# Kernel optimization log

Measured on AMD Instinct MI355X. Metric: run time of the kernel, lower is better.

## Reference

```python
import jax, jax.numpy as jnp
import numpy as np

NB, B, C, L = 4, 16, 256, 4096
BN_EPS = 1e-5


def setup_inputs() -> dict:
    key = jax.random.key(0)
    ks = jax.random.split(key, 10)
    s = 0.02
    return {
        "x": jax.random.normal(ks[0], (NB, B, C, L), jnp.float32),
        "Wq": jax.random.normal(ks[1], (NB, C, C), jnp.float32) * s,
        "bq": jax.random.normal(ks[2], (NB, C), jnp.float32) * s,
        "Wk": jax.random.normal(ks[3], (NB, C, C), jnp.float32) * s,
        "bk": jax.random.normal(ks[4], (NB, C), jnp.float32) * s,
        "Wv": jax.random.normal(ks[5], (NB, C, C), jnp.float32) * s,
        "bv": jax.random.normal(ks[6], (NB, C), jnp.float32) * s,
        "Wo": jax.random.normal(ks[7], (NB, C, C), jnp.float32) * s,
        "bo": jax.random.normal(ks[8], (NB, C), jnp.float32) * s,
        "gamma": jnp.ones((NB, C), jnp.float32),
        "beta": jnp.zeros((NB, C), jnp.float32),
        "edge_w": jnp.ones((NB, NB), jnp.float32),
        "branch_imp": jnp.ones((NB,), jnp.float32),
    }


def _proj(W, b, x):
    # 1x1 Conv1d == per-branch channel mixing: [nb,o,c] x [nb,B,c,L] -> [nb,B,o,L]
    return jnp.einsum('noc,nbcl->nbol', W, x) + b[:, None, :, None]


def reference(x, Wq, bq, Wk, bk, Wv, bv, Wo, bo, gamma, beta, edge_w, branch_imp):
    feat_dim = x.shape[2]
    scale = jnp.sqrt(jnp.asarray(feat_dim, x.dtype))
    q = _proj(Wq, bq, x)
    k = _proj(Wk, bk, x)
    v = _proj(Wv, bv, x)
    # descriptors: [nb, B, C, 2] = (mean over L, max over L)
    qd = jnp.stack([q.mean(axis=-1), q.max(axis=-1)], axis=-1)
    kd = jnp.stack([k.mean(axis=-1), k.max(axis=-1)], axis=-1)
    # mean over 2x2 bmm entries == (sum_p qd)(sum_q kd) summed over C, / 4
    scores = jnp.einsum('ibcp,jbcq->ijb', qd, kd) / (4.0 * scale)
    scores = scores * edge_w[:, :, None]
    attn = jax.nn.softmax(scores, axis=1) * jax.nn.softmax(branch_imp)[None, :, None]
    # weighted aggregation over source branches j
    agg = jnp.einsum('ijb,jbcl->ibcl', attn, v)
    out = _proj(Wo, bo, agg)
    # BatchNorm1d (training-mode batch statistics over B and L per channel, per branch)
    mean = out.mean(axis=(1, 3), keepdims=True)
    var = out.var(axis=(1, 3), keepdims=True)
    bn = (out - mean) * jax.lax.rsqrt(var + BN_EPS)
    bn = bn * gamma[:, None, :, None] + beta[:, None, :, None]
    return jax.nn.relu(bn) + x
```

## Files before the change

kernel.cpp:

```cpp
#include <hip/hip_runtime.h>
#include <stdint.h>
#include <stddef.h>

#define NBR 4
#define BSZ 16
#define CHN 256
#define LEN 4096
#define NB_B 64
#define BL   65536
#define BN_EPS 1e-5f
#define W_EL (NBR*CHN*CHN)

typedef unsigned short ushortT;
typedef unsigned short ushort4_t __attribute__((ext_vector_type(4)));
typedef unsigned short ushort8_t __attribute__((ext_vector_type(8)));
typedef short bf16x8 __attribute__((ext_vector_type(8)));
typedef float f32x4 __attribute__((ext_vector_type(4)));

__device__ __forceinline__ float bf2f(ushortT u) {
    return __uint_as_float(((unsigned)u) << 16);
}
__device__ __forceinline__ ushortT f2bf(float f) {
    unsigned b = __float_as_uint(f);
    return (ushortT)((b + 0x7FFFu + ((b >> 16) & 1u)) >> 16);
}
__device__ __forceinline__ unsigned encf(float f) {
    unsigned b = __float_as_uint(f);
    return (b & 0x80000000u) ? ~b : (b | 0x80000000u);
}
__device__ __forceinline__ float decf(unsigned u) {
    unsigned b = (u & 0x80000000u) ? (u ^ 0x80000000u) : ~u;
    return __uint_as_float(b);
}

__device__ __forceinline__ int swzX(int row, int cb) {
    return row * 512 + (cb ^ ((row & 7) << 4) ^ (((row >> 3) & 3) << 7));
}
__device__ __forceinline__ int swzW(int row, int cb) {
    return row * 128 + (cb ^ ((row & 7) << 4));
}

template <bool BF16IN>
__device__ __forceinline__ void stage_x(const void* act, ushortT* sX, int z, int lbase, int tid)
{
    const int ls = tid & 127;
    const int gh = tid >> 7;
    if (BF16IN) {
        const ushortT* xp = (const ushortT*)act + (size_t)z * CHN * LEN + lbase + ls;
#pragma unroll
        for (int g = 0; g < 16; ++g) {
            int c0 = (gh * 16 + g) * 8;
            ushort8_t u;
#pragma unroll
            for (int i = 0; i < 8; ++i) u[i] = xp[(size_t)(c0 + i) * LEN];
            *(ushort8_t*)((char*)sX + swzX(ls, c0 * 2)) = u;
        }
    } else {
        const float* xp = (const float*)act + (size_t)z * CHN * LEN + lbase + ls;
#pragma unroll
        for (int g = 0; g < 16; ++g) {
            int c0 = (gh * 16 + g) * 8;
            ushort8_t u;
#pragma unroll
            for (int i = 0; i < 8; ++i) u[i] = f2bf(xp[(size_t)(c0 + i) * LEN]);
            *(ushort8_t*)((char*)sX + swzX(ls, c0 * 2)) = u;
        }
    }
}

__device__ __forceinline__ void stage_w(const ushortT* Wb, ushortT* sW, int obase, int kb, int tid)
{
    const int r = tid >> 1;
    const int h = tid & 1;
    const ushortT* wp = Wb + (size_t)(obase + r) * CHN + kb + h * 32;
#pragma unroll
    for (int i = 0; i < 4; ++i) {
        ushort8_t u = *(const ushort8_t*)(wp + i * 8);
        *(ushort8_t*)((char*)sW + swzW(r, h * 64 + i * 16)) = u;
    }
}

__device__ __forceinline__ void mfma_chunk(const ushortT* sX, const ushortT* sW,
                                           f32x4 acc[4][4], int wr, int wc, int lane, int kb)
{
    const int am = wr * 64 + (lane & 15);
    const int bo = wc * 64 + (lane & 15);
    const int kg = (lane >> 4) * 16;
#pragma unroll
    for (int s = 0; s < 2; ++s) {
        bf16x8 a[4], b[4];
#pragma unroll
        for (int mf = 0; mf < 4; ++mf)
            a[mf] = *(const bf16x8*)((const char*)sX + swzX(am + mf * 16, kb * 2 + s * 64 + kg));
#pragma unroll
        for (int nf = 0; nf < 4; ++nf)
            b[nf] = *(const bf16x8*)((const char*)sW + swzW(bo + nf * 16, s * 64 + kg));
#pragma unroll
        for (int mf = 0; mf < 4; ++mf)
#pragma unroll
            for (int nf = 0; nf < 4; ++nf)
                acc[mf][nf] = __builtin_amdgcn_mfma_f32_16x16x32_bf16(a[mf], b[nf], acc[mf][nf], 0, 0, 0);
    }
}

__global__ __launch_bounds__(256, 2)
void qkv_kernel(const float* __restrict__ x, const ushortT* __restrict__ Wbf,
                const float* __restrict__ bv,
                float* __restrict__ qsum, unsigned* __restrict__ qmax,
                float* __restrict__ ksum, unsigned* __restrict__ kmax,
                ushortT* __restrict__ vbuf)
{
    __shared__ ushortT sX[128 * 256];
    __shared__ ushortT sW[128 * 64];
    const int tid = threadIdx.x;
    const int lane = tid & 63;
    const int wv = tid >> 6;
    const int wr = wv >> 1, wc = wv & 1;
    const int lbase = blockIdx.x * 128;
    const int z = blockIdx.y;
    const int n = z >> 4;

    stage_x<false>(x, sX, z, lbase, tid);

    for (int w = 0; w < 3; ++w) {
        const ushortT* Wb = Wbf + ((size_t)w * NBR + n) * CHN * CHN;
        for (int ot = 0; ot < 2; ++ot) {
            const int obase = ot * 128;
            f32x4 acc[4][4];
            const f32x4 z4 = {0.f, 0.f, 0.f, 0.f};
#pragma unroll
            for (int mf = 0; mf < 4; ++mf)
#pragma unroll
                for (int nf = 0; nf < 4; ++nf) acc[mf][nf] = z4;

            for (int kb = 0; kb < 4; ++kb) {
                __syncthreads();
                stage_w(Wb, sW, obase, kb * 64, tid);
                __syncthreads();
                mfma_chunk(sX, sW, acc, wr, wc, lane, kb * 64);
            }

            if (w < 2) {
                float* rs = (w == 0) ? qsum : ksum;
                unsigned* rm = (w == 0) ? qmax : kmax;
#pragma unroll
                for (int nf = 0; nf < 4; ++nf) {
                    float s = 0.f, m = -3.4e38f;
#pragma unroll
                    for (int mf = 0; mf < 4; ++mf)
#pragma unroll
                        for (int r = 0; r < 4; ++r) {
                            float v = acc[mf][nf][r];
                            s += v; m = fmaxf(m, v);
                        }
                    s += __shfl_xor(s, 16); s += __shfl_xor(s, 32);
                    m = fmaxf(m, __shfl_xor(m, 16)); m = fmaxf(m, __shfl_xor(m, 32));
                    if (lane < 16) {
                        int o = obase + wc * 64 + nf * 16 + lane;
                        atomicAdd(&rs[z * CHN + o], s);
                        atomicMax(&rm[z * CHN + o], encf(m));
                    }
                }
            } else {
#pragma unroll
                for (int nf = 0; nf < 4; ++nf) {
                    int o = obase + wc * 64 + nf * 16 + (lane & 15);
                    float bvv = bv[n * CHN + o];
#pragma unroll
                    for (int mf = 0; mf < 4; ++mf) {
                        int l = lbase + wr * 64 + mf * 16 + ((lane >> 4) << 2);
                        ushort4_t u;
#pragma unroll
                        for (int r = 0; r < 4; ++r) u[r] = f2bf(acc[mf][nf][r] + bvv);
                        *(ushort4_t*)(vbuf + (size_t)(z * CHN + o) * LEN + l) = u;
                    }
                }
            }
        }
    }
}

__global__ __launch_bounds__(256, 2)
void ogemm_kernel(const ushortT* __restrict__ agg, const ushortT* __restrict__ Wbo,
                  const float* __restrict__ bo_,
                  float* __restrict__ bnsum, float* __restrict__ bnss,
                  ushortT* __restrict__ outpre)
{
    __shared__ ushortT sX[128 * 256];
    __shared__ ushortT sW[128 * 64];
    const int tid = threadIdx.x;
    const int lane = tid & 63;
    const int wv = tid >> 6;
    const int wr = wv >> 1, wc = wv & 1;
    const int lbase = blockIdx.x * 128;
    const int z = blockIdx.y;
    const int n = z >> 4;
    const ushortT* Wb = Wbo + (size_t)n * CHN * CHN;

    stage_x<true>(agg, sX, z, lbase, tid);

    for (int ot = 0; ot < 2; ++ot) {
        const int obase = ot * 128;
        f32x4 acc[4][4];
        const f32x4 z4 = {0.f, 0.f, 0.f, 0.f};
#pragma unroll
        for (int mf = 0; mf < 4; ++mf)
#pragma unroll
            for (int nf = 0; nf < 4; ++nf) acc[mf][nf] = z4;

        for (int kb = 0; kb < 4; ++kb) {
            __syncthreads();
            stage_w(Wb, sW, obase, kb * 64, tid);
            __syncthreads();
            mfma_chunk(sX, sW, acc, wr, wc, lane, kb * 64);
        }

#pragma unroll
        for (int nf = 0; nf < 4; ++nf) {
            int o = obase + wc * 64 + nf * 16 + (lane & 15);
            float bb = bo_[n * CHN + o];
            float s = 0.f, q2 = 0.f;
#pragma unroll
            for (int mf = 0; mf < 4; ++mf) {
                int l = lbase + wr * 64 + mf * 16 + ((lane >> 4) << 2);
                ushort4_t u;
#pragma unroll
                for (int r = 0; r < 4; ++r) {
                    float v = acc[mf][nf][r] + bb;
                    u[r] = f2bf(v);
                    s += v; q2 += v * v;
                }
                *(ushort4_t*)(outpre + (size_t)(z * CHN + o) * LEN + l) = u;
            }
            s += __shfl_xor(s, 16); s += __shfl_xor(s, 32);
            q2 += __shfl_xor(q2, 16); q2 += __shfl_xor(q2, 32);
            if (lane < 16) {
                atomicAdd(&bnsum[n * CHN + o], s);
                atomicAdd(&bnss[n * CHN + o], q2);
            }
        }
    }
}

__global__ void wcvt_kernel(const float* __restrict__ Wq, const float* __restrict__ Wk,
                            const float* __restrict__ Wv, const float* __restrict__ Wo,
                            ushortT* __restrict__ Wbf)
{
    int t = blockIdx.x * 256 + threadIdx.x;
    const int per = W_EL / 4;
    if (t < 4 * per) {
        const float* srcs[4] = {Wq, Wk, Wv, Wo};
        int w = t / per;
        int r = t - w * per;
        float4 f = *(const float4*)(srcs[w] + (size_t)r * 4);
        ushort4_t u = {f2bf(f.x), f2bf(f.y), f2bf(f.z), f2bf(f.w)};
        *(ushort4_t*)(Wbf + (size_t)w * W_EL + (size_t)r * 4) = u;
    }
}

__global__ void attn_kernel(const float* __restrict__ qsum, const unsigned* __restrict__ qmax,
                            const float* __restrict__ ksum, const unsigned* __restrict__ kmax,
                            const float* __restrict__ bq, const float* __restrict__ bk,
                            const float* __restrict__ edge, const float* __restrict__ bimp,
                            float* __restrict__ attn)
{
    __shared__ float sc[NBR][NBR][BSZ];
    int tid = threadIdx.x;
    int i = tid >> 6, j = (tid >> 4) & 3, b = tid & 15;
    float s = 0.f;
    const float invL = 1.0f / (float)LEN;
    for (int c = 0; c < CHN; ++c) {
        int qi = (i * BSZ + b) * CHN + c;
        int ki = (j * BSZ + b) * CHN + c;
        float sq = qsum[qi] * invL + decf(qmax[qi]) + 2.f * bq[i * CHN + c];
        float sk = ksum[ki] * invL + decf(kmax[ki]) + 2.f * bk[j * CHN + c];
        s += sq * sk;
    }
    sc[i][j][b] = s * edge[i * 4 + j] * (1.0f / 64.0f);
    __syncthreads();
    if (tid < 64) {
        int ii = tid >> 4, bb = tid & 15;
        float m = -3.4e38f;
        for (int jj = 0; jj < 4; ++jj) m = fmaxf(m, sc[ii][jj][bb]);
        float e[4]; float sum = 0.f;
        for (int jj = 0; jj < 4; ++jj) { e[jj] = __expf(sc[ii][jj][bb] - m); sum += e[jj]; }
        float bm = fmaxf(fmaxf(bimp[0], bimp[1]), fmaxf(bimp[2], bimp[3]));
        float be[4]; float bs = 0.f;
        for (int jj = 0; jj < 4; ++jj) { be[jj] = __expf(bimp[jj] - bm); bs += be[jj]; }
        for (int jj = 0; jj < 4; ++jj)
            attn[(ii * 4 + jj) * BSZ + bb] = (e[jj] / sum) * (be[jj] / bs);
    }
}

__global__ __launch_bounds__(256)
void agg_kernel(const ushortT* __restrict__ v, const float* __restrict__ attn,
                ushortT* __restrict__ agg)
{
    __shared__ float sa[256];
    sa[threadIdx.x] = attn[threadIdx.x];
    __syncthreads();
    const long long U = (long long)BSZ * CHN * (LEN / 8);
    for (long long u = (long long)blockIdx.x * blockDim.x + threadIdx.x; u < U;
         u += (long long)gridDim.x * blockDim.x) {
        int l0 = (int)(u & 511) * 8;
        int c  = (int)(u >> 9) & 255;
        int b  = (int)(u >> 17);
        float vv[4][8];
#pragma unroll
        for (int j = 0; j < 4; ++j) {
            ushort8_t raw = *(const ushort8_t*)(v + (((size_t)(j * BSZ + b) * CHN + c) * LEN) + l0);
#pragma unroll
            for (int e = 0; e < 8; ++e) vv[j][e] = bf2f(raw[e]);
        }
#pragma unroll
        for (int i = 0; i < 4; ++i) {
            float a0 = sa[(i * 4 + 0) * BSZ + b];
            float a1 = sa[(i * 4 + 1) * BSZ + b];
            float a2 = sa[(i * 4 + 2) * BSZ + b];
            float a3 = sa[(i * 4 + 3) * BSZ + b];
            ushort8_t out;
#pragma unroll
            for (int e = 0; e < 8; ++e) {
                float r = a0 * vv[0][e] + a1 * vv[1][e] + a2 * vv[2][e] + a3 * vv[3][e];
                out[e] = f2bf(r);
            }
            *(ushort8_t*)(agg + (((size_t)(i * BSZ + b) * CHN + c) * LEN) + l0) = out;
        }
    }
}

__global__ void bnfin_kernel(const float* __restrict__ bnsum, const float* __restrict__ bnss,
                             const float* __restrict__ gamma, const float* __restrict__ beta,
                             float* __restrict__ scl, float* __restrict__ shf)
{
    int t = blockIdx.x * blockDim.x + threadIdx.x;
    if (t < NBR * CHN) {
        const float inv = 1.0f / (float)BL;
        float mean = bnsum[t] * inv;
        float var = bnss[t] * inv - mean * mean;
        float rs = rsqrtf(var + BN_EPS);
        float s = gamma[t] * rs;
        scl[t] = s;
        shf[t] = beta[t] - mean * s;
    }
}

__global__ __launch_bounds__(256)
void final_kernel(const ushortT* __restrict__ outpre, const float* __restrict__ x,
                  const float* __restrict__ scl, const float* __restrict__ shf,
                  float* __restrict__ out)
{
    const long long U = (long long)NB_B * CHN * (LEN / 8);
    for (long long u = (long long)blockIdx.x * blockDim.x + threadIdx.x; u < U;
         u += (long long)gridDim.x * blockDim.x) {
        int l0 = (int)(u & 511) * 8;
        int c  = (int)(u >> 9) & 255;
        int zz = (int)(u >> 17);
        int n  = zz >> 4;
        size_t base = ((size_t)zz * CHN + c) * LEN + l0;
        ushort8_t op = *(const ushort8_t*)(outpre + base);
        float4 x0 = *(const float4*)(x + base);
        float4 x1 = *(const float4*)(x + base + 4);
        float sc = scl[n * CHN + c];
        float sh = shf[n * CHN + c];
        float xr[8] = {x0.x, x0.y, x0.z, x0.w, x1.x, x1.y, x1.z, x1.w};
        float res[8];
#pragma unroll
        for (int e = 0; e < 8; ++e) {
            float bn = bf2f(op[e]) * sc + sh;
            res[e] = fmaxf(bn, 0.f) + xr[e];
        }
        float4 o0 = {res[0], res[1], res[2], res[3]};
        float4 o1 = {res[4], res[5], res[6], res[7]};
        *(float4*)(out + base) = o0;
        *(float4*)(out + base + 4) = o1;
    }
}

extern "C" void kernel_launch(void* const* d_in, const int* in_sizes, int n_in,
                              void* d_out, int out_size, void* d_ws, size_t ws_size,
                              hipStream_t stream)
{
    const float* x     = (const float*)d_in[0];
    const float* Wq    = (const float*)d_in[1];
    const float* bq    = (const float*)d_in[2];
    const float* Wk    = (const float*)d_in[3];
    const float* bk    = (const float*)d_in[4];
    const float* Wv    = (const float*)d_in[5];
    const float* bv    = (const float*)d_in[6];
    const float* Wo    = (const float*)d_in[7];
    const float* bo    = (const float*)d_in[8];
    const float* gamma = (const float*)d_in[9];
    const float* beta  = (const float*)d_in[10];
    const float* edge  = (const float*)d_in[11];
    const float* bimp  = (const float*)d_in[12];

    char* ws = (char*)d_ws;
    const size_t V_BYTES = (size_t)NBR * BSZ * CHN * LEN * 2;
    ushortT* vbuf = (ushortT*)ws;
    size_t off = V_BYTES;
    float*    qsum = (float*)(ws + off);    off += 65536;
    unsigned* qmax = (unsigned*)(ws + off); off += 65536;
    float*    ksum = (float*)(ws + off);    off += 65536;
    unsigned* kmax = (unsigned*)(ws + off); off += 65536;
    float*    attn = (float*)(ws + off);    off += 1024;
    float*    bnsum= (float*)(ws + off);    off += 4096;
    float*    bnss = (float*)(ws + off);    off += 4096;
    float*    scl  = (float*)(ws + off);    off += 4096;
    float*    shf  = (float*)(ws + off);    off += 4096;

    hipMemsetAsync(ws + V_BYTES, 0, off - V_BYTES, stream);

    ushortT* aggbuf = (ushortT*)d_out;
    float*   outf   = (float*)d_out;
    ushortT* Wbf = (ushortT*)((char*)d_out + ((size_t)134217728));

    wcvt_kernel<<<(4 * W_EL / 4 + 255) / 256, 256, 0, stream>>>(Wq, Wk, Wv, Wo, Wbf);

    dim3 gq(LEN / 128, NB_B);
    qkv_kernel<<<gq, 256, 0, stream>>>(x, Wbf, bv, qsum, qmax, ksum, kmax, vbuf);
    attn_kernel<<<1, 256, 0, stream>>>(qsum, qmax, ksum, kmax, bq, bk, edge, bimp, attn);
    agg_kernel<<<2048, 256, 0, stream>>>(vbuf, attn, aggbuf);
    ogemm_kernel<<<gq, 256, 0, stream>>>(aggbuf, Wbf + (size_t)3 * W_EL, bo, bnsum, bnss, vbuf);
    bnfin_kernel<<<4, 256, 0, stream>>>(bnsum, bnss, gamma, beta, scl, shf);
    final_kernel<<<8192, 256, 0, stream>>>(vbuf, x, scl, shf, outf);
}
```

Before: 560.7 us.

## Pre-pack weights into MFMA fragment layout and load B operands directly from global

The weight conversion kernel now writes bf16 weights in a per-lane MFMA fragment order, so each wave can load its B operands straight from global/L2 with contiguous 16-byte loads. The shared-memory weight staging and the two barriers per k-chunk in both GEMM kernels are removed, which also frees LDS. In exchange, every wave reads weights from global memory with no reuse through LDS, so the kernel relies on the cache hierarchy to absorb the repeated weight traffic.

```diff
diff --git a/kernel.cpp b/kernel.cpp
--- a/kernel.cpp
+++ b/kernel.cpp
@@ -36,65 +36,54 @@
 __device__ __forceinline__ int swzX(int row, int cb) {
     return row * 512 + (cb ^ ((row & 7) << 4) ^ (((row >> 3) & 3) << 7));
 }
-__device__ __forceinline__ int swzW(int row, int cb) {
-    return row * 128 + (cb ^ ((row & 7) << 4));
-}
-
-template <bool BF16IN>
-__device__ __forceinline__ void stage_x(const void* act, ushortT* sX, int z, int lbase, int tid)
+
+__device__ __forceinline__ void stage_x_f32(const float* x, ushortT* sX, int z, int lbase, int tid)
 {
     const int ls = tid & 127;
     const int gh = tid >> 7;
-    if (BF16IN) {
-        const ushortT* xp = (const ushortT*)act + (size_t)z * CHN * LEN + lbase + ls;
-#pragma unroll
-        for (int g = 0; g < 16; ++g) {
-            int c0 = (gh * 16 + g) * 8;
-            ushort8_t u;
-#pragma unroll
-            for (int i = 0; i < 8; ++i) u[i] = xp[(size_t)(c0 + i) * LEN];
-            *(ushort8_t*)((char*)sX + swzX(ls, c0 * 2)) = u;
-        }
-    } else {
-        const float* xp = (const float*)act + (size_t)z * CHN * LEN + lbase + ls;
-#pragma unroll
-        for (int g = 0; g < 16; ++g) {
-            int c0 = (gh * 16 + g) * 8;
-            ushort8_t u;
-#pragma unroll
-            for (int i = 0; i < 8; ++i) u[i] = f2bf(xp[(size_t)(c0 + i) * LEN]);
-            *(ushort8_t*)((char*)sX + swzX(ls, c0 * 2)) = u;
-        }
-    }
-}
-
-__device__ __forceinline__ void stage_w(const ushortT* Wb, ushortT* sW, int obase, int kb, int tid)
-{
-    const int r = tid >> 1;
-    const int h = tid & 1;
-    const ushortT* wp = Wb + (size_t)(obase + r) * CHN + kb + h * 32;
-#pragma unroll
-    for (int i = 0; i < 4; ++i) {
-        ushort8_t u = *(const ushort8_t*)(wp + i * 8);
-        *(ushort8_t*)((char*)sW + swzW(r, h * 64 + i * 16)) = u;
-    }
-}
-
-__device__ __forceinline__ void mfma_chunk(const ushortT* sX, const ushortT* sW,
-                                           f32x4 acc[4][4], int wr, int wc, int lane, int kb)
+    const float* xp = x + (size_t)z * CHN * LEN + lbase + ls;
+#pragma unroll
+    for (int g = 0; g < 16; ++g) {
+        int c0 = (gh * 16 + g) * 8;
+        ushort8_t u;
+#pragma unroll
+        for (int i = 0; i < 8; ++i) u[i] = f2bf(xp[(size_t)(c0 + i) * LEN]);
+        *(ushort8_t*)((char*)sX + swzX(ls, c0 * 2)) = u;
+    }
+}
+__device__ __forceinline__ void stage_x_bf16(const ushortT* a, ushortT* sX, int z, int lbase, int tid)
+{
+    const int ls = tid & 127;
+    const int gh = tid >> 7;
+    const ushortT* xp = a + (size_t)z * CHN * LEN + lbase + ls;
+#pragma unroll
+    for (int g = 0; g < 16; ++g) {
+        int c0 = (gh * 16 + g) * 8;
+        ushort8_t u;
+#pragma unroll
+        for (int i = 0; i < 8; ++i) u[i] = xp[(size_t)(c0 + i) * LEN];
+        *(ushort8_t*)((char*)sX + swzX(ls, c0 * 2)) = u;
+    }
+}
+
+__device__ __forceinline__ void mfma_chunk_frag(const ushortT* sX, const ushortT* __restrict__ Wb2,
+                                                int otile, f32x4 acc[4][4],
+                                                int wr, int wc, int lane, int kb)
 {
     const int am = wr * 64 + (lane & 15);
-    const int bo = wc * 64 + (lane & 15);
     const int kg = (lane >> 4) * 16;
 #pragma unroll
     for (int s = 0; s < 2; ++s) {
+        const int cb = kb * 2 + s;
         bf16x8 a[4], b[4];
 #pragma unroll
+        for (int nf = 0; nf < 4; ++nf) {
+            const int ob = otile * 8 + wc * 4 + nf;
+            b[nf] = *(const bf16x8*)(Wb2 + (((size_t)ob * 8 + cb) * 64 + lane) * 8);
+        }
+#pragma unroll
         for (int mf = 0; mf < 4; ++mf)
-            a[mf] = *(const bf16x8*)((const char*)sX + swzX(am + mf * 16, kb * 2 + s * 64 + kg));
-#pragma unroll
-        for (int nf = 0; nf < 4; ++nf)
-            b[nf] = *(const bf16x8*)((const char*)sW + swzW(bo + nf * 16, s * 64 + kg));
+            a[mf] = *(const bf16x8*)((const char*)sX + swzX(am + mf * 16, kb * 128 + s * 64 + kg));
 #pragma unroll
         for (int mf = 0; mf < 4; ++mf)
 #pragma unroll
@@ -111,7 +100,6 @@
                 ushortT* __restrict__ vbuf)
 {
     __shared__ ushortT sX[128 * 256];
-    __shared__ ushortT sW[128 * 64];
     const int tid = threadIdx.x;
     const int lane = tid & 63;
     const int wv = tid >> 6;
@@ -120,26 +108,24 @@
     const int z = blockIdx.y;
     const int n = z >> 4;
 
-    stage_x<false>(x, sX, z, lbase, tid);
+    stage_x_f32(x, sX, z, lbase, tid);
+    __syncthreads();
+
+    const f32x4 z4 = {0.f, 0.f, 0.f, 0.f};
 
     for (int w = 0; w < 3; ++w) {
-        const ushortT* Wb = Wbf + ((size_t)w * NBR + n) * CHN * CHN;
+        const ushortT* Wb2 = Wbf + ((size_t)w * NBR + n) * CHN * CHN;
         for (int ot = 0; ot < 2; ++ot) {
+            f32x4 acc[4][4];
+#pragma unroll
+            for (int mf = 0; mf < 4; ++mf)
+#pragma unroll
+                for (int nf = 0; nf < 4; ++nf) acc[mf][nf] = z4;
+#pragma unroll
+            for (int kb = 0; kb < 4; ++kb)
+                mfma_chunk_frag(sX, Wb2, ot, acc, wr, wc, lane, kb);
+
             const int obase = ot * 128;
-            f32x4 acc[4][4];
-            const f32x4 z4 = {0.f, 0.f, 0.f, 0.f};
-#pragma unroll
-            for (int mf = 0; mf < 4; ++mf)
-#pragma unroll
-                for (int nf = 0; nf < 4; ++nf) acc[mf][nf] = z4;
-
-            for (int kb = 0; kb < 4; ++kb) {
-                __syncthreads();
-                stage_w(Wb, sW, obase, kb * 64, tid);
-                __syncthreads();
-                mfma_chunk(sX, sW, acc, wr, wc, lane, kb * 64);
-            }
-
             if (w < 2) {
                 float* rs = (w == 0) ? qsum : ksum;
                 unsigned* rm = (w == 0) ? qmax : kmax;
@@ -187,7 +173,6 @@
                   ushortT* __restrict__ outpre)
 {
     __shared__ ushortT sX[128 * 256];
-    __shared__ ushortT sW[128 * 64];
     const int tid = threadIdx.x;
     const int lane = tid & 63;
     const int wv = tid >> 6;
@@ -195,26 +180,23 @@
     const int lbase = blockIdx.x * 128;
     const int z = blockIdx.y;
     const int n = z >> 4;
-    const ushortT* Wb = Wbo + (size_t)n * CHN * CHN;
-
-    stage_x<true>(agg, sX, z, lbase, tid);
-
+    const ushortT* Wb2 = Wbo + (size_t)n * CHN * CHN;
+
+    stage_x_bf16(agg, sX, z, lbase, tid);
+    __syncthreads();
+
+    const f32x4 z4 = {0.f, 0.f, 0.f, 0.f};
     for (int ot = 0; ot < 2; ++ot) {
+        f32x4 acc[4][4];
+#pragma unroll
+        for (int mf = 0; mf < 4; ++mf)
+#pragma unroll
+            for (int nf = 0; nf < 4; ++nf) acc[mf][nf] = z4;
+#pragma unroll
+        for (int kb = 0; kb < 4; ++kb)
+            mfma_chunk_frag(sX, Wb2, ot, acc, wr, wc, lane, kb);
+
         const int obase = ot * 128;
-        f32x4 acc[4][4];
-        const f32x4 z4 = {0.f, 0.f, 0.f, 0.f};
-#pragma unroll
-        for (int mf = 0; mf < 4; ++mf)
-#pragma unroll
-            for (int nf = 0; nf < 4; ++nf) acc[mf][nf] = z4;
-
-        for (int kb = 0; kb < 4; ++kb) {
-            __syncthreads();
-            stage_w(Wb, sW, obase, kb * 64, tid);
-            __syncthreads();
-            mfma_chunk(sX, sW, acc, wr, wc, lane, kb * 64);
-        }
-
 #pragma unroll
         for (int nf = 0; nf < 4; ++nf) {
             int o = obase + wc * 64 + nf * 16 + (lane & 15);
@@ -247,14 +229,23 @@
                             ushortT* __restrict__ Wbf)
 {
     int t = blockIdx.x * 256 + threadIdx.x;
-    const int per = W_EL / 4;
-    if (t < 4 * per) {
+    if (t < 4 * (W_EL / 8)) {
         const float* srcs[4] = {Wq, Wk, Wv, Wo};
-        int w = t / per;
-        int r = t - w * per;
-        float4 f = *(const float4*)(srcs[w] + (size_t)r * 4);
-        ushort4_t u = {f2bf(f.x), f2bf(f.y), f2bf(f.z), f2bf(f.w)};
-        *(ushort4_t*)(Wbf + (size_t)w * W_EL + (size_t)r * 4) = u;
+        int w    = t >> 15;
+        int r    = t & 32767;
+        int lane = r & 63;
+        int cb   = (r >> 6) & 7;
+        int ob   = (r >> 9) & 15;
+        int n    = r >> 13;
+        const float* src = srcs[w] + (size_t)n * CHN * CHN;
+        int o = ob * 16 + (lane & 15);
+        int c = cb * 32 + (lane >> 4) * 8;
+        float4 f0 = *(const float4*)(src + (size_t)o * CHN + c);
+        float4 f1 = *(const float4*)(src + (size_t)o * CHN + c + 4);
+        ushort8_t u = {f2bf(f0.x), f2bf(f0.y), f2bf(f0.z), f2bf(f0.w),
+                       f2bf(f1.x), f2bf(f1.y), f2bf(f1.z), f2bf(f1.w)};
+        *(ushort8_t*)(Wbf + ((size_t)w * NBR + n) * CHN * CHN
+                          + (((size_t)ob * 8 + cb) * 64 + lane) * 8) = u;
     }
 }
 
@@ -412,10 +403,10 @@
     hipMemsetAsync(ws + V_BYTES, 0, off - V_BYTES, stream);
 
     ushortT* aggbuf = (ushortT*)d_out;
-    float*   outf   = (float*)d_out;
     ushortT* Wbf = (ushortT*)((char*)d_out + ((size_t)134217728));
-
-    wcvt_kernel<<<(4 * W_EL / 4 + 255) / 256, 256, 0, stream>>>(Wq, Wk, Wv, Wo, Wbf);
+    float*   outf = (float*)d_out;
+
+    wcvt_kernel<<<(4 * (W_EL / 8) + 255) / 256, 256, 0, stream>>>(Wq, Wk, Wv, Wo, Wbf);
 
     dim3 gq(LEN / 128, NB_B);
     qkv_kernel<<<gq, 256, 0, stream>>>(x, Wbf, bv, qsum, qmax, ksum, kmax, vbuf);
```

Measured after the change: 521.6 us. 7.0% less time.
